# Performance work log

Measured on AMD Instinct MI355X. Metric: run time of the kernel, lower is better.

Reference implementation:

```python
import jax, jax.numpy as jnp
import numpy as np
from jax import lax

N_CLASSES = 10
GTG_ITER = 30
GTG_TOL = 1e-3
PLB = 0.5
EPS = 1e-8
B = 4096
INTERM = 128
CHANNELS = [64, 128, 256, 512]
SIZES = [8, 8, 4, 4]
EMB_DIM = 512


def setup_inputs() -> dict:
    key = jax.random.key(0)
    ks = jax.random.split(key, 16)
    inp = {}
    for i, (c, s) in enumerate(zip(CHANNELS, SIZES)):
        inp[f"feat{i}"] = jax.random.normal(ks[i], (B, c, s, s), dtype=jnp.float32)
    inp["embedds"] = jax.random.normal(ks[4], (B, EMB_DIM), dtype=jnp.float32)
    inp["outs"] = jax.random.normal(ks[5], (B, N_CLASSES), dtype=jnp.float32)
    inp["labels"] = jax.random.randint(ks[6], (B,), 0, N_CLASSES)
    for i, c in enumerate(CHANNELS):
        inp[f"ls_w{i}"] = jax.random.normal(ks[7 + i], (c, INTERM), dtype=jnp.float32) / np.sqrt(c).astype(np.float32)
        inp[f"ls_b{i}"] = jnp.zeros((INTERM,), dtype=jnp.float32)
    in_feat = GTG_ITER * N_CLASSES  # 300
    inp["mlp_w1"] = jax.random.normal(ks[11], (in_feat, in_feat // 2), dtype=jnp.float32) / np.sqrt(in_feat).astype(np.float32)
    inp["mlp_b1"] = jnp.zeros((in_feat // 2,), dtype=jnp.float32)
    inp["mlp_w2"] = jax.random.normal(ks[12], (in_feat // 2, in_feat // 4), dtype=jnp.float32) / np.sqrt(in_feat // 2).astype(np.float32)
    inp["mlp_b2"] = jnp.zeros((in_feat // 4,), dtype=jnp.float32)
    inp["mlp_w3"] = jax.random.normal(ks[13], (in_feat // 4 * 4, 1), dtype=jnp.float32) / np.sqrt(in_feat).astype(np.float32)
    inp["mlp_b3"] = jnp.zeros((1,), dtype=jnp.float32)
    return inp


def _make_A(emb):
    # get_A_cos_sim: normalize -> NN^T -> zero diag -> clamp[0,1]
    n = emb / jnp.maximum(jnp.linalg.norm(emb, axis=-1, keepdims=True), 1e-12)
    A = n @ n.T
    A = A * (1.0 - jnp.eye(A.shape[0], dtype=A.dtype))
    A = jnp.clip(A, 0.0, 1.0)
    # threshold strategy 'mean': zero entries below mean(A)
    A = jnp.where(A < jnp.mean(A), 0.0, A)
    # AM_strategy 'diversity': A = 1 - A
    return 1.0 - A


def _gtg(A, X0):
    # graph transduction game; while-loop emulated via scan with a running flag
    def step(carry, _):
        X, running = carry
        mult = X * (A @ X)                                 # [B,C]
        div = mult / (jnp.sum(mult, axis=1, keepdims=True) + EPS)
        X_new = X + div
        div_d = lax.stop_gradient(div)
        ent = -jnp.sum(div_d * jnp.log(div_d + EPS), axis=1)  # entropy, detached
        err = jnp.linalg.norm(div_d - lax.stop_gradient(X))
        X_out = jnp.where(running, X_new, X)
        xs_t = jnp.where(running, X_new, jnp.zeros_like(X_new))
        ent_t = jnp.where(running, ent, jnp.zeros_like(ent))
        return (X_out, jnp.logical_and(running, err > GTG_TOL)), (xs_t, ent_t)

    (_, _), (Xs, ents) = lax.scan(step, (X0, jnp.array(True)), None, length=GTG_ITER)
    return jnp.transpose(Xs, (1, 2, 0)), ents.T  # [B,C,T], [B,T]


def _ls(feat, w, b):
    # AvgPool2d over full spatial + Linear + ReLU
    pooled = jnp.mean(feat, axis=(2, 3))  # [B, n_c]
    return jax.nn.relu(pooled @ w + b)


def _mlp(xs_list, w1, b1, w2, b2, w3, b3):
    outs = []
    for xs in xs_list:
        x = xs.reshape(xs.shape[0], -1)  # [B, C*T], torch .view order
        x = jax.nn.relu(x @ w1 + b1)
        x = jax.nn.relu(x @ w2 + b2)
        outs.append(x)
    return (jnp.concatenate(outs, axis=1) @ w3 + b3)[:, 0]


def _init_X(labels, batch):
    n_lab = int(batch * PLB)
    X0 = jnp.full((batch, N_CLASSES), 1.0 / N_CLASSES, dtype=jnp.float32)
    X0 = X0.at[:n_lab].set(0.0)
    X0 = X0.at[jnp.arange(n_lab), labels[:n_lab]].set(1.0)
    return X0, n_lab


def reference(feat0, feat1, feat2, feat3, embedds, outs, labels,
              ls_w0, ls_b0, ls_w1, ls_b1, ls_w2, ls_b2, ls_w3, ls_b3,
              mlp_w1, mlp_b1, mlp_w2, mlp_b2, mlp_w3, mlp_b3):
    batch = embedds.shape[0]
    X0, n_lab = _init_X(labels, batch)
    feats = [feat0, feat1, feat2, feat3]
    lws = [ls_w0, ls_w1, ls_w2, ls_w3]
    lbs = [ls_b0, ls_b1, ls_b2, ls_b3]
    xs_list = []
    for f, w, b in zip(feats, lws, lbs):
        emb = _ls(f, w, b)
        Xs, _ = _gtg(_make_A(emb), X0)
        xs_list.append(Xs)
    y_pred = _mlp(xs_list, mlp_w1, mlp_b1, mlp_w2, mlp_b2, mlp_w3, mlp_b3)  # [B]
    _, ents = _gtg(_make_A(embedds), X0)
    y_true = jnp.mean(ents, axis=1)  # ent_strategy 'mean'
    labelled_mask = jnp.arange(batch) < n_lab
    return y_pred, y_true, labelled_mask
```

## Files before the change

### kernel.cpp

```cpp
#include <hip/hip_runtime.h>
#include <hip/hip_fp16.h>

typedef _Float16 f16x8 __attribute__((ext_vector_type(8)));
typedef float f32x4 __attribute__((ext_vector_type(4)));
typedef unsigned char uchar;

static __device__ __forceinline__ long long mk64(unsigned lo, unsigned hi)
{
    return (long long)(((unsigned long long)hi << 32) | (unsigned long long)lo);
}

static __device__ __forceinline__ int xfrag_off(int c, int j)
{
    return (j >> 6) * 1024 + (((j >> 3) & 3) * 16 + c) * 16 + ((j >> 5) & 1) * 8 + (j & 7);
}

static __device__ __forceinline__ int xsfrag_off(int row, int k)
{
    return (row >> 4) * 5120 + (k >> 5) * 512 + (((k >> 3) & 3) * 16 + (row & 15)) * 8 + (k & 7);
}

#define T03 0x24201800u
#define T47 0x2E2C2A28u
#define T8B 0x33323130u
#define TCF 0x37363534u

static __device__ __forceinline__ void expand4(unsigned w, unsigned& o0, unsigned& o1)
{
    unsigned even = w & 0x0F0F0F0Fu;
    unsigned odd  = (w >> 4) & 0x0F0F0F0Fu;
    unsigned i_lo = __builtin_amdgcn_perm(odd, even, 0x05010400u);
    unsigned i_hi = __builtin_amdgcn_perm(odd, even, 0x07030602u);
    {
        unsigned i3 = i_lo & 0x07070707u;
        unsigned ta = __builtin_amdgcn_perm(T47, T03, i3);
        unsigned tb = __builtin_amdgcn_perm(TCF, T8B, i3);
        unsigned m  = ((i_lo >> 3) & 0x01010101u) * 0xFFu;
        o0 = ta ^ ((ta ^ tb) & m);
    }
    {
        unsigned i3 = i_hi & 0x07070707u;
        unsigned ta = __builtin_amdgcn_perm(T47, T03, i3);
        unsigned tb = __builtin_amdgcn_perm(TCF, T8B, i3);
        unsigned m  = ((i_hi >> 3) & 0x01010101u) * 0xFFu;
        o1 = ta ^ ((ta ^ tb) & m);
    }
}

template <int S2>
__global__ __launch_bounds__(256) void pool_kernel(const float* __restrict__ feat,
                                                   float* __restrict__ pooled, int total)
{
    int idx = blockIdx.x * 256 + threadIdx.x;
    if (idx >= total) return;
    const float4* p4 = (const float4*)(feat + (size_t)idx * S2);
    float s = 0.f;
#pragma unroll
    for (int i = 0; i < S2 / 4; ++i) {
        float4 v = p4[i];
        s += v.x + v.y + v.z + v.w;
    }
    pooled[idx] = s * (1.0f / S2);
}

__global__ __launch_bounds__(128) void ls_norm_kernel(const float* __restrict__ pooled,
                                                      const float* __restrict__ w,
                                                      const float* __restrict__ bias,
                                                      __half* __restrict__ n16, int K)
{
    __shared__ float pl[512];
    __shared__ float red2[2];
    const int b = blockIdx.x, t = threadIdx.x;
    for (int k = t; k < K; k += 128) pl[k] = pooled[(size_t)b * K + k];
    __syncthreads();
    float acc = bias[t];
    for (int k = 0; k < K; ++k) acc = fmaf(pl[k], w[(size_t)k * 128 + t], acc);
    float v = fmaxf(acc, 0.f);
    float ss = v * v;
    for (int off = 32; off > 0; off >>= 1) ss += __shfl_down(ss, off, 64);
    if ((t & 63) == 0) red2[t >> 6] = ss;
    __syncthreads();
    float inv = 1.0f / fmaxf(sqrtf(red2[0] + red2[1]), 1e-12f);
    n16[(size_t)b * 128 + t] = __float2half(v * inv);
}

__global__ __launch_bounds__(256) void norm512_kernel(const float* __restrict__ E,
                                                      __half* __restrict__ n16)
{
    __shared__ float red4[4];
    const int b = blockIdx.x, t = threadIdx.x;
    float2 v = *(const float2*)(E + (size_t)b * 512 + t * 2);
    float ss = v.x * v.x + v.y * v.y;
    for (int off = 32; off > 0; off >>= 1) ss += __shfl_down(ss, off, 64);
    if ((t & 63) == 0) red4[t >> 6] = ss;
    __syncthreads();
    float inv = 1.0f / fmaxf(sqrtf(red4[0] + red4[1] + red4[2] + red4[3]), 1e-12f);
    __half2 o;
    o.x = __float2half(v.x * inv);
    o.y = __float2half(v.y * inv);
    *(__half2*)(n16 + (size_t)b * 512 + t * 2) = o;
}

template <int K>
__global__ __launch_bounds__(256) void a_gemm_core(const __half* __restrict__ N16,
                                                   __half* __restrict__ A16f,
                                                   float* __restrict__ partials)
{
    __shared__ __half smem[16384];
    __shared__ float reds[4];
    __half* As = smem;
    __half* Bs = smem + 8192;
    char* Cb = (char*)smem;
    const int t = threadIdx.x;
    const int lane = t & 63, wave = t >> 6;
    const int bx = blockIdx.x & 31, by = blockIdx.x >> 5;
    const int wr = wave >> 1, wc = wave & 1;
    const int fr = lane & 15;
    const int g = lane >> 4;
    const int r0 = by * 128, c0 = bx * 128;
    const int sr = t >> 3;
    const int sc = t & 7;

    f32x4 acc[4][4];
#pragma unroll
    for (int i = 0; i < 4; ++i)
#pragma unroll
        for (int j = 0; j < 4; ++j) acc[i][j] = (f32x4){0.f, 0.f, 0.f, 0.f};

    for (int kt = 0; kt < K / 64; ++kt) {
        const int kb = kt * 64;
        __syncthreads();
#pragma unroll
        for (int pp = 0; pp < 4; ++pp) {
            const int r = pp * 32 + sr;
            uint4 va = *(const uint4*)(N16 + (size_t)(r0 + r) * K + kb + sc * 8);
            uint4 vb = *(const uint4*)(N16 + (size_t)(c0 + r) * K + kb + sc * 8);
            const int d = r * 64 + ((((sc * 16) ^ ((r & 7) << 4))) >> 1);
            *(uint4*)&As[d] = va;
            *(uint4*)&Bs[d] = vb;
        }
        __syncthreads();
#pragma unroll
        for (int ks = 0; ks < 2; ++ks) {
            const int ko = ((ks * 64 + g * 16) ^ ((fr & 7) << 4)) >> 1;
            f16x8 af[4], bf[4];
#pragma unroll
            for (int i = 0; i < 4; ++i) {
                af[i] = *(const f16x8*)&As[(wr * 64 + i * 16 + fr) * 64 + ko];
                bf[i] = *(const f16x8*)&Bs[(wc * 64 + i * 16 + fr) * 64 + ko];
            }
#pragma unroll
            for (int i = 0; i < 4; ++i)
#pragma unroll
                for (int j = 0; j < 4; ++j)
                    acc[i][j] = __builtin_amdgcn_mfma_f32_16x16x32_f16(af[i], bf[j], acc[i][j], 0, 0, 0);
        }
    }
    __syncthreads();

    float lsum = 0.f;
    const int r4 = g * 4;
#pragma unroll
    for (int i = 0; i < 4; ++i) {
#pragma unroll
        for (int q = 0; q < 4; ++q) {
            const int lr = wr * 64 + i * 16 + r4 + q;
            const int row = r0 + lr;
#pragma unroll
            for (int j = 0; j < 4; ++j) {
                const int lc = wc * 64 + j * 16 + fr;
                const int col = c0 + lc;
                float v = fminf(fmaxf(acc[i][j][q], 0.f), 1.f);
                if (row == col) v = 0.f;
                lsum += v;
                *(__half*)(Cb + lr * 256 + ((lc * 2) ^ ((lr & 7) << 4))) = __float2half(v);
            }
        }
    }
    __syncthreads();

#pragma unroll
    for (int pp = 0; pp < 4; ++pp) {
        const int rbl2 = pp * 4 + (t >> 6);
        const int rbl = rbl2 >> 1, ks2l = rbl2 & 1;
        const int l = t & 63;
        const int lr = rbl * 16 + (l & 15);
        const int e0 = ks2l * 64 + (l >> 4) * 8;
        uint4 v0 = *(const uint4*)(Cb + lr * 256 + ((e0 * 2) ^ ((lr & 7) << 4)));
        uint4 v1 = *(const uint4*)(Cb + lr * 256 + (((e0 + 32) * 2) ^ ((lr & 7) << 4)));
        const size_t rb = (size_t)(by * 8 + rbl);
        const size_t ks2 = (size_t)(bx * 2 + ks2l);
        char* dst = (char*)A16f + rb * 131072 + ks2 * 2048 + l * 32;
        *(uint4*)dst = v0;
        *(uint4*)(dst + 16) = v1;
    }

    for (int off = 32; off > 0; off >>= 1) lsum += __shfl_down(lsum, off, 64);
    if (lane == 0) reds[wave] = lsum;
    __syncthreads();
    if (t == 0) partials[blockIdx.x] = reds[0] + reds[1] + reds[2] + reds[3];
}

__global__ __launch_bounds__(256) void mean_kernel(const float* __restrict__ partials,
                                                   float* __restrict__ scal)
{
    __shared__ float red[4];
    const int t = threadIdx.x;
    float s = 0.f;
    for (int i = t; i < 1024; i += 256) s += partials[i];
    for (int off = 32; off > 0; off >>= 1) s += __shfl_down(s, off, 64);
    if ((t & 63) == 0) red[t >> 6] = s;
    __syncthreads();
    if (t == 0) scal[0] = (red[0] + red[1] + red[2] + red[3]) * (1.0f / 16777216.0f);
}

__global__ __launch_bounds__(256) void abar4_frag_kernel(const __half* __restrict__ A16f,
                                                         uchar* __restrict__ A4,
                                                         const float* __restrict__ scal)
{
    const float mean = scal[0];
    const size_t i = ((size_t)blockIdx.x * 256 + threadIdx.x);
    uint4 u0 = *(const uint4*)(A16f + i * 16);
    uint4 u1 = *(const uint4*)(A16f + i * 16 + 8);
    __half h[16];
    *(uint4*)h = u0;
    *(uint4*)(h + 8) = u1;
    unsigned d0 = 0, d1 = 0;
#pragma unroll
    for (int k = 0; k < 8; ++k) {
        float a = __half2float(h[k]);
        float v = (a < mean) ? 0.f : a;
        unsigned n = (unsigned)fminf(v * 16.f + 0.5f, 15.f);
        d0 |= n << (4 * k);
    }
#pragma unroll
    for (int k = 0; k < 8; ++k) {
        float a = __half2float(h[8 + k]);
        float v = (a < mean) ? 0.f : a;
        unsigned n = (unsigned)fminf(v * 16.f + 0.5f, 15.f);
        d1 |= n << (4 * k);
    }
    uint2 o; o.x = d0; o.y = d1;
    *(uint2*)(A4 + i * 8) = o;
}

__global__ __launch_bounds__(256) void scol0_kernel(const int* __restrict__ labels,
                                                    float* __restrict__ Scol)
{
    __shared__ int hist[16];
    const int t = threadIdx.x;
    if (t < 16) hist[t] = 0;
    __syncthreads();
    for (int i = t; i < 2048; i += 256) atomicAdd(&hist[labels[i]], 1);
    __syncthreads();
    if (t < 80) {
        const int p = t >> 4, c = t & 15;
        Scol[p * 16 + c] = (c < 10) ? ((float)hist[c] + 204.8f) : 0.f;
    }
}

__global__ __launch_bounds__(256) void init_kernel(const int* __restrict__ labels,
                                                   uchar* __restrict__ X8_0,
                                                   uchar* __restrict__ X8_1,
                                                   float* __restrict__ X32)
{
    const int idx = blockIdx.x * 256 + threadIdx.x;
    const int p = idx >> 16;
    const int rem = idx & 65535;
    const int c = rem >> 12, j = rem & 4095;
    float v;
    if (c >= 10) v = 0.f;
    else if (j < 2048) v = (labels[j] == c) ? 1.0f : 0.0f;
    else v = 0.1f;
    unsigned pk = __builtin_amdgcn_cvt_pk_fp8_f32(v, v, 0, false);
    X8_0[(size_t)p * 65536 + xfrag_off(c, j)] = (uchar)(pk & 0xff);
    if (c >= 10) X8_1[(size_t)p * 65536 + xfrag_off(c, j)] = 0;
    if (c < 10) X32[((size_t)p * 4096 + j) * 10 + c] = v;
}

__global__ __launch_bounds__(256) void wfrag_kernel(const float* __restrict__ w1,
                                                    const float* __restrict__ w2,
                                                    __half* __restrict__ W1f,
                                                    __half* __restrict__ W2f)
{
    int idx = blockIdx.x * 256 + threadIdx.x;
    if (idx < 51200) {
        const int frag = idx >> 9, e9 = idx & 511;
        const int s = frag / 10, j = frag % 10;
        const int g = e9 >> 7, fr = (e9 >> 3) & 15, e = e9 & 7;
        const int k = s * 32 + g * 8 + e, n = j * 16 + fr;
        const float v = (k < 300 && n < 150) ? w1[(size_t)k * 150 + n] : 0.f;
        W1f[idx] = __float2half(v);
    } else if (idx < 64000) {
        const int i2 = idx - 51200;
        const int frag = i2 >> 9, e9 = i2 & 511;
        const int s = frag / 5, j = frag % 5;
        const int g = e9 >> 7, fr = (e9 >> 3) & 15, e = e9 & 7;
        const int k = s * 32 + g * 8 + e, n = j * 16 + fr;
        const float v = (k < 150 && n < 75) ? w2[(size_t)k * 75 + n] : 0.f;
        W2f[i2] = __float2half(v);
    }
}

__global__ __launch_bounds__(256, 4) void gtg8_kernel(
    const uchar* __restrict__ A4f,
    const uchar* __restrict__ X8i, uchar* __restrict__ X8o,
    const float* __restrict__ X32i, float* __restrict__ X32o,
    __half* __restrict__ Xs16f, float* __restrict__ ytacc,
    float* __restrict__ Scol, int it, int pbase)
{
    __shared__ float yred[4][256];
    const int t = threadIdx.x;
    const int lane = t & 63, wave = t >> 6;
    const int p = pbase + (blockIdx.x >> 8);
    const int pl = p - pbase;
    const int rb = blockIdx.x & 255;

    const uchar* Ab = A4f + (size_t)pl * 8388608 + (size_t)rb * 32768
                    + wave * 8192 + lane * 8;
    const uchar* Xb = X8i + (size_t)p * 65536 + wave * 16384 + lane * 16;

    f32x4 acc0 = {0.f, 0.f, 0.f, 0.f};
    f32x4 acc1 = {0.f, 0.f, 0.f, 0.f};
#pragma unroll
    for (int u = 0; u < 16; ++u) {
        uint2 a4 = *(const uint2*)(Ab + u * 512);
        uint4 bv = *(const uint4*)(Xb + u * 1024);
        unsigned e00, e01, e10, e11;
        expand4(a4.x, e00, e01);
        expand4(a4.y, e10, e11);
        acc0 = __builtin_amdgcn_mfma_f32_16x16x32_fp8_fp8(
            mk64(e00, e01), mk64(bv.x, bv.y), acc0, 0, 0, 0);
        acc1 = __builtin_amdgcn_mfma_f32_16x16x32_fp8_fp8(
            mk64(e10, e11), mk64(bv.z, bv.w), acc1, 0, 0, 0);
    }
    {
        const int r4 = (lane >> 4) * 4;
        const int fr = lane & 15;
#pragma unroll
        for (int q = 0; q < 4; ++q)
            yred[wave][(r4 + q) * 16 + fr] = acc0[q] + acc1[q];
    }
    __syncthreads();

    const int r = t >> 4, c = t & 15;
    const int row = rb * 16 + r;
    const float T = yred[0][t] + yred[1][t] + yred[2][t] + yred[3][t];
    const float y = Scol[it * 80 + pl * 16 + c] - T;
    const float x = (c < 10) ? X32i[((size_t)p * 4096 + row) * 10 + c] : 0.f;
    const float m = x * y;
    float s = m;
    s += __shfl_xor(s, 1, 16);
    s += __shfl_xor(s, 2, 16);
    s += __shfl_xor(s, 4, 16);
    s += __shfl_xor(s, 8, 16);
    const float dv = m / (s + 1e-8f);
    const float xn = x + dv;
    if (c < 10) {
        X32o[((size_t)p * 4096 + row) * 10 + c] = xn;
        unsigned pk = __builtin_amdgcn_cvt_pk_fp8_f32(xn, xn, 0, false);
        X8o[(size_t)p * 65536 + xfrag_off(c, row)] = (uchar)(pk & 0xff);
        if (p < 4) {
            const int k = c * 30 + it;
            Xs16f[(size_t)p * 1310720 + xsfrag_off(row, k)] = __float2half(xn);
        }
    }
    if (p == 4) {
        float e = (c < 10) ? (-dv * logf(dv + 1e-8f)) : 0.f;
        e += __shfl_xor(e, 1, 16);
        e += __shfl_xor(e, 2, 16);
        e += __shfl_xor(e, 4, 16);
        e += __shfl_xor(e, 8, 16);
        if (c == 0) {
            float prev = (it == 0) ? 0.f : ytacc[row];
            ytacc[row] = prev + e;
        }
    }

    __syncthreads();
    yred[0][t] = (c < 10) ? xn : 0.f;
    __syncthreads();
    if (t < 10) {
        float sc = 0.f;
#pragma unroll
        for (int rr = 0; rr < 16; ++rr) sc += yred[0][t + rr * 16];
        atomicAdd(&Scol[(it + 1) * 80 + pl * 16 + t], sc);
    }
}

__global__ __launch_bounds__(256) void mlp_mfma_kernel(const __half* __restrict__ Xs16f,
                                                       const __half* __restrict__ W1f,
                                                       const __half* __restrict__ W2f,
                                                       const float* __restrict__ b1,
                                                       const float* __restrict__ b2,
                                                       float* __restrict__ H2)
{
    __shared__ char h1s[4][16 * 384];
    __shared__ float b1s[160];
    __shared__ float b2s[80];
    const int t = threadIdx.x;
    const int lane = t & 63, wave = t >> 6;
    const int fr = lane & 15, g = lane >> 4;
    const int lvl = blockIdx.x >> 6;
    const int rb = (blockIdx.x & 63) * 4 + wave;

    if (t < 160) b1s[t] = (t < 150) ? b1[t] : 0.f;
    else if (t < 240) b2s[t - 160] = (t < 235) ? b2[t - 160] : 0.f;
    __syncthreads();

    const __half* Abase = Xs16f + (size_t)lvl * 1310720 + (size_t)rb * 5120;
    f32x4 acc1[10];
#pragma unroll
    for (int j = 0; j < 10; ++j) acc1[j] = (f32x4){0.f, 0.f, 0.f, 0.f};
#pragma unroll
    for (int s = 0; s < 10; ++s) {
        f16x8 a = *(const f16x8*)(Abase + s * 512 + lane * 8);
#pragma unroll
        for (int j = 0; j < 10; ++j) {
            f16x8 b = *(const f16x8*)(W1f + (s * 10 + j) * 512 + lane * 8);
            acc1[j] = __builtin_amdgcn_mfma_f32_16x16x32_f16(a, b, acc1[j], 0, 0, 0);
        }
    }
    char* hw = h1s[wave];
#pragma unroll
    for (int j = 0; j < 10; ++j) {
#pragma unroll
        for (int q = 0; q < 4; ++q) {
            const int row = g * 4 + q;
            const int col = j * 16 + fr;
            float v = fmaxf(acc1[j][q] + b1s[col], 0.f);
            *(__half*)(hw + row * 384 + ((col * 2) ^ ((row & 7) << 4))) = __float2half(v);
        }
    }
    __syncthreads();

    f32x4 acc2[5];
#pragma unroll
    for (int j = 0; j < 5; ++j) acc2[j] = (f32x4){0.f, 0.f, 0.f, 0.f};
#pragma unroll
    for (int s = 0; s < 5; ++s) {
        f16x8 a = *(const f16x8*)(hw + fr * 384 + ((s * 64 + g * 16) ^ ((fr & 7) << 4)));
#pragma unroll
        for (int j = 0; j < 5; ++j) {
            f16x8 b = *(const f16x8*)(W2f + (s * 5 + j) * 512 + lane * 8);
            acc2[j] = __builtin_amdgcn_mfma_f32_16x16x32_f16(a, b, acc2[j], 0, 0, 0);
        }
    }
#pragma unroll
    for (int j = 0; j < 5; ++j) {
        const int col = j * 16 + fr;
        if (col < 75) {
#pragma unroll
            for (int q = 0; q < 4; ++q) {
                const int row = rb * 16 + g * 4 + q;
                float v = fmaxf(acc2[j][q] + b2s[col], 0.f);
                H2[(size_t)row * 300 + lvl * 75 + col] = v;
            }
        }
    }
}

__global__ __launch_bounds__(256) void final_kernel(const float* __restrict__ H2,
                                                    const float* __restrict__ w3,
                                                    const float* __restrict__ b3,
                                                    const float* __restrict__ ytacc,
                                                    float* __restrict__ out)
{
    __shared__ float w[300];
    const int t = threadIdx.x;
    const int b = blockIdx.x * 256 + t;
    for (int i = t; i < 300; i += 256) w[i] = w3[i];
    __syncthreads();
    float acc = b3[0];
    const float4* row = (const float4*)(H2 + (size_t)b * 300);
    for (int k4 = 0; k4 < 75; ++k4) {
        float4 v = row[k4];
        acc += v.x * w[k4 * 4] + v.y * w[k4 * 4 + 1] + v.z * w[k4 * 4 + 2] + v.w * w[k4 * 4 + 3];
    }
    out[b] = acc;
    out[4096 + b] = ytacc[b] * (1.0f / 30.0f);
    out[2 * 4096 + b] = (b < 2048) ? 1.0f : 0.0f;
}

extern "C" void kernel_launch(void* const* d_in, const int* in_sizes, int n_in,
                              void* d_out, int out_size, void* d_ws, size_t ws_size,
                              hipStream_t stream)
{
    (void)in_sizes; (void)n_in; (void)out_size;

    const float* feats[4] = {(const float*)d_in[0], (const float*)d_in[1],
                             (const float*)d_in[2], (const float*)d_in[3]};
    const float* embedds = (const float*)d_in[4];
    const int* labels = (const int*)d_in[6];
    const float* lsw[4] = {(const float*)d_in[7], (const float*)d_in[9],
                           (const float*)d_in[11], (const float*)d_in[13]};
    const float* lsb[4] = {(const float*)d_in[8], (const float*)d_in[10],
                           (const float*)d_in[12], (const float*)d_in[14]};
    const float* w1 = (const float*)d_in[15];
    const float* b1 = (const float*)d_in[16];
    const float* w2 = (const float*)d_in[17];
    const float* b2 = (const float*)d_in[18];
    const float* w3 = (const float*)d_in[19];
    const float* b3 = (const float*)d_in[20];

    const bool fused = ws_size >= 156930304ULL;
    const size_t A4_BYTES = fused ? 41943040ULL : 8388608ULL;

    char* ws = (char*)d_ws;
    uchar* A4       = (uchar*)(ws);
    __half* A16f    = (__half*)(ws + A4_BYTES);
    char* base      = ws + A4_BYTES + 33554432;
    float* pooled   = (float*)(base);
    __half* N16     = (__half*)(base + 8388608);
    uchar* Xt8      = (uchar*)(base + 12582912);
    float* X32      = (float*)(base + 13238272);
    __half* Xs16f   = (__half*)(base + 14876672);
    float* H2       = (float*)(base + 25362432);
    float* ytacc    = (float*)(base + 30277632);
    float* partials = (float*)(base + 30294016);
    float* scal     = (float*)(base + 30298112);
    float* Scol     = (float*)(base + 30298368);
    __half* W1f     = (__half*)(base + 30314752);
    __half* W2f     = (__half*)(base + 30417152);

    uchar* Xt8b[2] = {Xt8, Xt8 + 327680};
    float* X32b[2] = {X32, X32 + 204800};
    float* out = (float*)d_out;

    const int Cs[4] = {64, 128, 256, 512};
    const int S2s[4] = {64, 64, 16, 16};

    auto run_iters = [&](const uchar* Ab4, int pbase, int nprob) {
        hipMemsetAsync(Scol, 0, 31 * 80 * sizeof(float), stream);
        if (pbase == 0) hipMemsetAsync(Xs16f, 0, 10485760, stream);
        scol0_kernel<<<1, 256, 0, stream>>>(labels, Scol);
        init_kernel<<<1280, 256, 0, stream>>>(labels, Xt8b[0], Xt8b[1], X32b[0]);
        for (int it = 0; it < 30; ++it) {
            const int i = it & 1, o = i ^ 1;
            gtg8_kernel<<<nprob * 256, 256, 0, stream>>>(
                Ab4, Xt8b[i], Xt8b[o], X32b[i], X32b[o], Xs16f, ytacc, Scol, it, pbase);
        }
    };

    wfrag_kernel<<<250, 256, 0, stream>>>(w1, w2, W1f, W2f);

    for (int lvl = 0; lvl < 4; ++lvl) {
        const int c = Cs[lvl];
        const int total = 4096 * c;
        if (S2s[lvl] == 64)
            pool_kernel<64><<<total / 256, 256, 0, stream>>>(feats[lvl], pooled, total);
        else
            pool_kernel<16><<<total / 256, 256, 0, stream>>>(feats[lvl], pooled, total);
        ls_norm_kernel<<<4096, 128, 0, stream>>>(pooled, lsw[lvl], lsb[lvl], N16, c);
        uchar* Ab4 = A4 + (fused ? (size_t)lvl * 8388608 : 0);
        a_gemm_core<128><<<1024, 256, 0, stream>>>(N16, A16f, partials);
        mean_kernel<<<1, 256, 0, stream>>>(partials, scal);
        abar4_frag_kernel<<<4096, 256, 0, stream>>>(A16f, Ab4, scal);
        if (!fused) {
            run_iters(Ab4, lvl, 1);
        }
    }

    norm512_kernel<<<4096, 256, 0, stream>>>(embedds, N16);
    {
        uchar* Ab4 = A4 + (fused ? (size_t)4 * 8388608 : 0);
        a_gemm_core<512><<<1024, 256, 0, stream>>>(N16, A16f, partials);
        mean_kernel<<<1, 256, 0, stream>>>(partials, scal);
        abar4_frag_kernel<<<4096, 256, 0, stream>>>(A16f, Ab4, scal);
        if (!fused) run_iters(Ab4, 4, 1);
    }

    if (fused) run_iters(A4, 0, 5);
    mlp_mfma_kernel<<<256, 256, 0, stream>>>(Xs16f, W1f, W2f, b1, b2, H2);

    final_kernel<<<16, 256, 0, stream>>>(H2, w3, b3, ytacc, out);
}
```

Measured before the change: 824.7 us.

## Batch all five similarity-matrix problems into single fused preprocessing and GEMM launches

Pooling, the linear-ReLU layer and L2 normalisation for all four feature levels and the embedding are merged into one kernel, indexed by problem. The A-matrix GEMM, mean and 4-bit quantisation kernels then each run as one launch over all five problems. The Scol histogram setup and its memset are folded into init_kernel, and gtg8_kernel's launch bound goes from 4 to 5 blocks per SM. This cuts many small serial launches and lets the GEMMs fill the GPU together, at the cost of a much larger fp16 A workspace. The fused path now needs a bigger workspace threshold, so if the workspace is too small the code falls back to the slower per-problem GTG path.

```diff
diff --git a/kernel.cpp b/kernel.cpp
--- a/kernel.cpp
+++ b/kernel.cpp
@@ -47,64 +47,101 @@
     }
 }
 
-template <int S2>
-__global__ __launch_bounds__(256) void pool_kernel(const float* __restrict__ feat,
-                                                   float* __restrict__ pooled, int total)
-{
-    int idx = blockIdx.x * 256 + threadIdx.x;
-    if (idx >= total) return;
-    const float4* p4 = (const float4*)(feat + (size_t)idx * S2);
-    float s = 0.f;
-#pragma unroll
-    for (int i = 0; i < S2 / 4; ++i) {
-        float4 v = p4[i];
-        s += v.x + v.y + v.z + v.w;
-    }
-    pooled[idx] = s * (1.0f / S2);
-}
-
-__global__ __launch_bounds__(128) void ls_norm_kernel(const float* __restrict__ pooled,
-                                                      const float* __restrict__ w,
-                                                      const float* __restrict__ bias,
-                                                      __half* __restrict__ n16, int K)
+__global__ __launch_bounds__(256) void fused_ls_kernel(
+    const float* __restrict__ f0, const float* __restrict__ f1,
+    const float* __restrict__ f2, const float* __restrict__ f3,
+    const float* __restrict__ embedds,
+    const float* __restrict__ lw0, const float* __restrict__ lb0,
+    const float* __restrict__ lw1, const float* __restrict__ lb1,
+    const float* __restrict__ lw2, const float* __restrict__ lb2,
+    const float* __restrict__ lw3, const float* __restrict__ lb3,
+    __half* __restrict__ N16all, int pbase)
 {
     __shared__ float pl[512];
-    __shared__ float red2[2];
-    const int b = blockIdx.x, t = threadIdx.x;
-    for (int k = t; k < K; k += 128) pl[k] = pooled[(size_t)b * K + k];
-    __syncthreads();
-    float acc = bias[t];
-    for (int k = 0; k < K; ++k) acc = fmaf(pl[k], w[(size_t)k * 128 + t], acc);
-    float v = fmaxf(acc, 0.f);
-    float ss = v * v;
-    for (int off = 32; off > 0; off >>= 1) ss += __shfl_down(ss, off, 64);
-    if ((t & 63) == 0) red2[t >> 6] = ss;
-    __syncthreads();
-    float inv = 1.0f / fmaxf(sqrtf(red2[0] + red2[1]), 1e-12f);
-    n16[(size_t)b * 128 + t] = __float2half(v * inv);
-}
-
-__global__ __launch_bounds__(256) void norm512_kernel(const float* __restrict__ E,
-                                                      __half* __restrict__ n16)
-{
-    __shared__ float red4[4];
-    const int b = blockIdx.x, t = threadIdx.x;
-    float2 v = *(const float2*)(E + (size_t)b * 512 + t * 2);
-    float ss = v.x * v.x + v.y * v.y;
-    for (int off = 32; off > 0; off >>= 1) ss += __shfl_down(ss, off, 64);
-    if ((t & 63) == 0) red4[t >> 6] = ss;
-    __syncthreads();
-    float inv = 1.0f / fmaxf(sqrtf(red4[0] + red4[1] + red4[2] + red4[3]), 1e-12f);
-    __half2 o;
-    o.x = __float2half(v.x * inv);
-    o.y = __float2half(v.y * inv);
-    *(__half2*)(n16 + (size_t)b * 512 + t * 2) = o;
-}
-
-template <int K>
-__global__ __launch_bounds__(256) void a_gemm_core(const __half* __restrict__ N16,
-                                                   __half* __restrict__ A16f,
-                                                   float* __restrict__ partials)
+    __shared__ float red[4];
+    const int t = threadIdx.x;
+    const int p = pbase + (blockIdx.x >> 12);
+    const int row = blockIdx.x & 4095;
+
+    if (p == 4) {
+        float2 v = *(const float2*)(embedds + (size_t)row * 512 + t * 2);
+        float ss = v.x * v.x + v.y * v.y;
+        for (int off = 32; off > 0; off >>= 1) ss += __shfl_down(ss, off, 64);
+        if ((t & 63) == 0) red[t >> 6] = ss;
+        __syncthreads();
+        float inv = 1.0f / fmaxf(sqrtf(red[0] + red[1] + red[2] + red[3]), 1e-12f);
+        __half2 o;
+        o.x = __float2half(v.x * inv);
+        o.y = __float2half(v.y * inv);
+        *(__half2*)(N16all + 2097152 + (size_t)row * 512 + t * 2) = o;
+        return;
+    }
+
+    const float* feat; const float* w; const float* b; int C;
+    switch (p) {
+        case 0:  feat = f0; w = lw0; b = lb0; C = 64;  break;
+        case 1:  feat = f1; w = lw1; b = lb1; C = 128; break;
+        case 2:  feat = f2; w = lw2; b = lb2; C = 256; break;
+        default: feat = f3; w = lw3; b = lb3; C = 512; break;
+    }
+    const float* fr = feat + (size_t)row * C * ((p < 2) ? 64 : 16);
+
+    if (p == 0) {
+        const int c = t >> 2, q = t & 3;
+        const float4* src = (const float4*)(fr + c * 64 + q * 16);
+        float s = 0.f;
+#pragma unroll
+        for (int i = 0; i < 4; ++i) { float4 v = src[i]; s += v.x + v.y + v.z + v.w; }
+        s += __shfl_xor(s, 1, 64);
+        s += __shfl_xor(s, 2, 64);
+        if (q == 0) pl[c] = s * (1.0f / 64.f);
+    } else if (p == 1) {
+        const int c = t >> 1, h = t & 1;
+        const float4* src = (const float4*)(fr + c * 64 + h * 32);
+        float s = 0.f;
+#pragma unroll
+        for (int i = 0; i < 8; ++i) { float4 v = src[i]; s += v.x + v.y + v.z + v.w; }
+        s += __shfl_xor(s, 1, 64);
+        if (h == 0) pl[c] = s * (1.0f / 64.f);
+    } else if (p == 2) {
+        const float4* src = (const float4*)(fr + t * 16);
+        float s = 0.f;
+#pragma unroll
+        for (int i = 0; i < 4; ++i) { float4 v = src[i]; s += v.x + v.y + v.z + v.w; }
+        pl[t] = s * (1.0f / 16.f);
+    } else {
+#pragma unroll
+        for (int cc = 0; cc < 2; ++cc) {
+            const int c = t + cc * 256;
+            const float4* src = (const float4*)(fr + c * 16);
+            float s = 0.f;
+#pragma unroll
+            for (int i = 0; i < 4; ++i) { float4 v = src[i]; s += v.x + v.y + v.z + v.w; }
+            pl[c] = s * (1.0f / 16.f);
+        }
+    }
+    __syncthreads();
+
+    float v = 0.f, ss = 0.f;
+    if (t < 128) {
+        float acc = b[t];
+        for (int k = 0; k < C; ++k) acc = fmaf(pl[k], w[(size_t)k * 128 + t], acc);
+        v = fmaxf(acc, 0.f);
+        ss = v * v;
+        for (int off = 32; off > 0; off >>= 1) ss += __shfl_down(ss, off, 64);
+        if ((t & 63) == 0) red[t >> 6] = ss;
+    }
+    __syncthreads();
+    if (t < 128) {
+        float inv = 1.0f / fmaxf(sqrtf(red[0] + red[1]), 1e-12f);
+        N16all[(size_t)p * 524288 + (size_t)row * 128 + t] = __float2half(v * inv);
+    }
+}
+
+__global__ __launch_bounds__(256) void a_gemm_all(const __half* __restrict__ N16all,
+                                                  __half* __restrict__ A16f,
+                                                  float* __restrict__ partials,
+                                                  int pbase)
 {
     __shared__ __half smem[16384];
     __shared__ float reds[4];
@@ -113,7 +150,12 @@
     char* Cb = (char*)smem;
     const int t = threadIdx.x;
     const int lane = t & 63, wave = t >> 6;
-    const int bx = blockIdx.x & 31, by = blockIdx.x >> 5;
+    const int lp = blockIdx.x >> 10;
+    const int p = pbase + lp;
+    const int blk = blockIdx.x & 1023;
+    const int K = (p == 4) ? 512 : 128;
+    const __half* N16 = N16all + ((p == 4) ? 2097152u : (unsigned)p * 524288u);
+    const int bx = blk & 31, by = blk >> 5;
     const int wr = wave >> 1, wc = wave & 1;
     const int fr = lane & 15;
     const int g = lane >> 4;
@@ -127,7 +169,7 @@
 #pragma unroll
         for (int j = 0; j < 4; ++j) acc[i][j] = (f32x4){0.f, 0.f, 0.f, 0.f};
 
-    for (int kt = 0; kt < K / 64; ++kt) {
+    for (int kt = 0; kt < (K >> 6); ++kt) {
         const int kb = kt * 64;
         __syncthreads();
 #pragma unroll
@@ -190,7 +232,7 @@
         uint4 v1 = *(const uint4*)(Cb + lr * 256 + (((e0 + 32) * 2) ^ ((lr & 7) << 4)));
         const size_t rb = (size_t)(by * 8 + rbl);
         const size_t ks2 = (size_t)(bx * 2 + ks2l);
-        char* dst = (char*)A16f + rb * 131072 + ks2 * 2048 + l * 32;
+        char* dst = (char*)A16f + (size_t)lp * 33554432 + rb * 131072 + ks2 * 2048 + l * 32;
         *(uint4*)dst = v0;
         *(uint4*)(dst + 16) = v1;
     }
@@ -198,30 +240,32 @@
     for (int off = 32; off > 0; off >>= 1) lsum += __shfl_down(lsum, off, 64);
     if (lane == 0) reds[wave] = lsum;
     __syncthreads();
-    if (t == 0) partials[blockIdx.x] = reds[0] + reds[1] + reds[2] + reds[3];
-}
-
-__global__ __launch_bounds__(256) void mean_kernel(const float* __restrict__ partials,
-                                                   float* __restrict__ scal)
+    if (t == 0) partials[lp * 1024 + blk] = reds[0] + reds[1] + reds[2] + reds[3];
+}
+
+__global__ __launch_bounds__(256) void mean_all_kernel(const float* __restrict__ partials,
+                                                       float* __restrict__ scal)
 {
     __shared__ float red[4];
-    const int t = threadIdx.x;
+    const int t = threadIdx.x, lp = blockIdx.x;
     float s = 0.f;
-    for (int i = t; i < 1024; i += 256) s += partials[i];
+    for (int i = t; i < 1024; i += 256) s += partials[lp * 1024 + i];
     for (int off = 32; off > 0; off >>= 1) s += __shfl_down(s, off, 64);
     if ((t & 63) == 0) red[t >> 6] = s;
     __syncthreads();
-    if (t == 0) scal[0] = (red[0] + red[1] + red[2] + red[3]) * (1.0f / 16777216.0f);
-}
-
-__global__ __launch_bounds__(256) void abar4_frag_kernel(const __half* __restrict__ A16f,
-                                                         uchar* __restrict__ A4,
-                                                         const float* __restrict__ scal)
-{
-    const float mean = scal[0];
-    const size_t i = ((size_t)blockIdx.x * 256 + threadIdx.x);
-    uint4 u0 = *(const uint4*)(A16f + i * 16);
-    uint4 u1 = *(const uint4*)(A16f + i * 16 + 8);
+    if (t == 0) scal[lp] = (red[0] + red[1] + red[2] + red[3]) * (1.0f / 16777216.0f);
+}
+
+__global__ __launch_bounds__(256) void abar4_all_kernel(const __half* __restrict__ A16f,
+                                                        uchar* __restrict__ A4,
+                                                        const float* __restrict__ scal)
+{
+    const int lp = blockIdx.x >> 12;
+    const float mean = scal[lp];
+    const size_t i = (size_t)(blockIdx.x & 4095) * 256 + threadIdx.x;
+    const __half* src = A16f + (size_t)lp * 16777216 + i * 16;
+    uint4 u0 = *(const uint4*)(src);
+    uint4 u1 = *(const uint4*)(src + 8);
     __half h[16];
     *(uint4*)h = u0;
     *(uint4*)(h + 8) = u1;
@@ -241,30 +285,19 @@
         d1 |= n << (4 * k);
     }
     uint2 o; o.x = d0; o.y = d1;
-    *(uint2*)(A4 + i * 8) = o;
-}
-
-__global__ __launch_bounds__(256) void scol0_kernel(const int* __restrict__ labels,
-                                                    float* __restrict__ Scol)
-{
-    __shared__ int hist[16];
-    const int t = threadIdx.x;
-    if (t < 16) hist[t] = 0;
-    __syncthreads();
-    for (int i = t; i < 2048; i += 256) atomicAdd(&hist[labels[i]], 1);
-    __syncthreads();
-    if (t < 80) {
-        const int p = t >> 4, c = t & 15;
-        Scol[p * 16 + c] = (c < 10) ? ((float)hist[c] + 204.8f) : 0.f;
-    }
+    *(uint2*)(A4 + (size_t)lp * 8388608 + i * 8) = o;
 }
 
 __global__ __launch_bounds__(256) void init_kernel(const int* __restrict__ labels,
                                                    uchar* __restrict__ X8_0,
                                                    uchar* __restrict__ X8_1,
-                                                   float* __restrict__ X32)
-{
-    const int idx = blockIdx.x * 256 + threadIdx.x;
+                                                   float* __restrict__ X32,
+                                                   float* __restrict__ Scol)
+{
+    __shared__ int hist[16];
+    const int blk = blockIdx.x;
+    const int t = threadIdx.x;
+    const int idx = blk * 256 + t;
     const int p = idx >> 16;
     const int rem = idx & 65535;
     const int c = rem >> 12, j = rem & 4095;
@@ -276,6 +309,19 @@
     X8_0[(size_t)p * 65536 + xfrag_off(c, j)] = (uchar)(pk & 0xff);
     if (c >= 10) X8_1[(size_t)p * 65536 + xfrag_off(c, j)] = 0;
     if (c < 10) X32[((size_t)p * 4096 + j) * 10 + c] = v;
+
+    if (blk == 0) {
+        if (t < 16) hist[t] = 0;
+        __syncthreads();
+        for (int i = t; i < 2048; i += 256) atomicAdd(&hist[labels[i]], 1);
+        __syncthreads();
+        if (t < 80) {
+            const int pp = t >> 4, cc = t & 15;
+            Scol[pp * 16 + cc] = (cc < 10) ? ((float)hist[cc] + 204.8f) : 0.f;
+        }
+    } else if (blk <= 30) {
+        if (t < 80) Scol[blk * 80 + t] = 0.f;
+    }
 }
 
 __global__ __launch_bounds__(256) void wfrag_kernel(const float* __restrict__ w1,
@@ -302,7 +348,7 @@
     }
 }
 
-__global__ __launch_bounds__(256, 4) void gtg8_kernel(
+__global__ __launch_bounds__(256, 5) void gtg8_kernel(
     const uchar* __restrict__ A4f,
     const uchar* __restrict__ X8i, uchar* __restrict__ X8o,
     const float* __restrict__ X32i, float* __restrict__ X32o,
@@ -503,38 +549,32 @@
     const float* w3 = (const float*)d_in[19];
     const float* b3 = (const float*)d_in[20];
 
-    const bool fused = ws_size >= 156930304ULL;
-    const size_t A4_BYTES = fused ? 41943040ULL : 8388608ULL;
+    const bool fused = ws_size >= 236000000ULL;
+    const size_t A4_BYTES  = fused ? 41943040ULL : 8388608ULL;
+    const size_t A16_BYTES = fused ? 167772160ULL : 33554432ULL;
 
     char* ws = (char*)d_ws;
     uchar* A4       = (uchar*)(ws);
     __half* A16f    = (__half*)(ws + A4_BYTES);
-    char* base      = ws + A4_BYTES + 33554432;
-    float* pooled   = (float*)(base);
-    __half* N16     = (__half*)(base + 8388608);
-    uchar* Xt8      = (uchar*)(base + 12582912);
-    float* X32      = (float*)(base + 13238272);
-    __half* Xs16f   = (__half*)(base + 14876672);
-    float* H2       = (float*)(base + 25362432);
-    float* ytacc    = (float*)(base + 30277632);
-    float* partials = (float*)(base + 30294016);
-    float* scal     = (float*)(base + 30298112);
-    float* Scol     = (float*)(base + 30298368);
-    __half* W1f     = (__half*)(base + 30314752);
-    __half* W2f     = (__half*)(base + 30417152);
+    char* base      = ws + A4_BYTES + A16_BYTES;
+    __half* N16all  = (__half*)(base);
+    uchar* Xt8      = (uchar*)(base + 8388608);
+    float* X32      = (float*)(base + 9043968);
+    __half* Xs16f   = (__half*)(base + 10682368);
+    float* H2       = (float*)(base + 21168128);
+    float* ytacc    = (float*)(base + 26083328);
+    float* partials = (float*)(base + 26099712);
+    float* scal     = (float*)(base + 26120192);
+    float* Scol     = (float*)(base + 26120448);
+    __half* W1f     = (__half*)(base + 26136832);
+    __half* W2f     = (__half*)(base + 26239232);
 
     uchar* Xt8b[2] = {Xt8, Xt8 + 327680};
     float* X32b[2] = {X32, X32 + 204800};
     float* out = (float*)d_out;
 
-    const int Cs[4] = {64, 128, 256, 512};
-    const int S2s[4] = {64, 64, 16, 16};
-
     auto run_iters = [&](const uchar* Ab4, int pbase, int nprob) {
-        hipMemsetAsync(Scol, 0, 31 * 80 * sizeof(float), stream);
-        if (pbase == 0) hipMemsetAsync(Xs16f, 0, 10485760, stream);
-        scol0_kernel<<<1, 256, 0, stream>>>(labels, Scol);
-        init_kernel<<<1280, 256, 0, stream>>>(labels, Xt8b[0], Xt8b[1], X32b[0]);
+        init_kernel<<<1280, 256, 0, stream>>>(labels, Xt8b[0], Xt8b[1], X32b[0], Scol);
         for (int it = 0; it < 30; ++it) {
             const int i = it & 1, o = i ^ 1;
             gtg8_kernel<<<nprob * 256, 256, 0, stream>>>(
@@ -543,35 +583,30 @@
     };
 
     wfrag_kernel<<<250, 256, 0, stream>>>(w1, w2, W1f, W2f);
-
-    for (int lvl = 0; lvl < 4; ++lvl) {
-        const int c = Cs[lvl];
-        const int total = 4096 * c;
-        if (S2s[lvl] == 64)
-            pool_kernel<64><<<total / 256, 256, 0, stream>>>(feats[lvl], pooled, total);
-        else
-            pool_kernel<16><<<total / 256, 256, 0, stream>>>(feats[lvl], pooled, total);
-        ls_norm_kernel<<<4096, 128, 0, stream>>>(pooled, lsw[lvl], lsb[lvl], N16, c);
-        uchar* Ab4 = A4 + (fused ? (size_t)lvl * 8388608 : 0);
-        a_gemm_core<128><<<1024, 256, 0, stream>>>(N16, A16f, partials);
-        mean_kernel<<<1, 256, 0, stream>>>(partials, scal);
-        abar4_frag_kernel<<<4096, 256, 0, stream>>>(A16f, Ab4, scal);
-        if (!fused) {
-            run_iters(Ab4, lvl, 1);
-        }
-    }
-
-    norm512_kernel<<<4096, 256, 0, stream>>>(embedds, N16);
-    {
-        uchar* Ab4 = A4 + (fused ? (size_t)4 * 8388608 : 0);
-        a_gemm_core<512><<<1024, 256, 0, stream>>>(N16, A16f, partials);
-        mean_kernel<<<1, 256, 0, stream>>>(partials, scal);
-        abar4_frag_kernel<<<4096, 256, 0, stream>>>(A16f, Ab4, scal);
-        if (!fused) run_iters(Ab4, 4, 1);
-    }
-
-    if (fused) run_iters(A4, 0, 5);
+    hipMemsetAsync(Xs16f, 0, 10485760, stream);
+
+    if (fused) {
+        fused_ls_kernel<<<5 * 4096, 256, 0, stream>>>(
+            feats[0], feats[1], feats[2], feats[3], embedds,
+            lsw[0], lsb[0], lsw[1], lsb[1], lsw[2], lsb[2], lsw[3], lsb[3],
+            N16all, 0);
+        a_gemm_all<<<5 * 1024, 256, 0, stream>>>(N16all, A16f, partials, 0);
+        mean_all_kernel<<<5, 256, 0, stream>>>(partials, scal);
+        abar4_all_kernel<<<5 * 4096, 256, 0, stream>>>(A16f, A4, scal);
+        run_iters(A4, 0, 5);
+    } else {
+        for (int p = 0; p < 5; ++p) {
+            fused_ls_kernel<<<4096, 256, 0, stream>>>(
+                feats[0], feats[1], feats[2], feats[3], embedds,
+                lsw[0], lsb[0], lsw[1], lsb[1], lsw[2], lsb[2], lsw[3], lsb[3],
+                N16all, p);
+            a_gemm_all<<<1024, 256, 0, stream>>>(N16all, A16f, partials, p);
+            mean_all_kernel<<<1, 256, 0, stream>>>(partials, scal);
+            abar4_all_kernel<<<4096, 256, 0, stream>>>(A16f, A4, scal);
+            run_iters(A4, p, 1);
+        }
+    }
+
     mlp_mfma_kernel<<<256, 256, 0, stream>>>(Xs16f, W1f, W2f, b1, b2, H2);
-
     final_kernel<<<16, 256, 0, stream>>>(H2, w3, b3, ytacc, out);
 }
```

Result: faster. 770.5 us (-6.6%).
